# Kernel tuning notes

Measured on AMD Instinct MI355X. Metric: run time of the kernel, lower is better.

The kernel has to match this reference:

```python
import jax, jax.numpy as jnp
import numpy as np
from jax import lax

DIM = 256
NUM_HEADS = 8
HEAD_DIM = DIM // NUM_HEADS
SCALE = HEAD_DIM ** -0.5


def _avg_pool(x, k, p):
    # torch AvgPool2d(kernel=k, stride=1, padding=p) with count_include_pad=True
    s = lax.reduce_window(x, 0.0, lax.add,
                          window_dimensions=(1, 1, k, k),
                          window_strides=(1, 1, 1, 1),
                          padding=((0, 0), (0, 0), (p, p), (p, p)))
    return s / (k * k)


def setup_inputs() -> dict:
    key = jax.random.key(0)
    ks = jax.random.split(key, 7)
    x = jax.random.normal(ks[0], (2, DIM, 48, 48), dtype=jnp.float32)
    q_w = jax.random.normal(ks[1], (DIM, DIM), dtype=jnp.float32) * (DIM ** -0.5)
    q_b = jax.random.normal(ks[2], (DIM,), dtype=jnp.float32) * 0.02
    kv_w = jax.random.normal(ks[3], (2 * DIM, DIM), dtype=jnp.float32) * (DIM ** -0.5)
    kv_b = jax.random.normal(ks[4], (2 * DIM,), dtype=jnp.float32) * 0.02
    proj_w = jax.random.normal(ks[5], (DIM, DIM), dtype=jnp.float32) * (DIM ** -0.5)
    proj_b = jax.random.normal(ks[6], (DIM,), dtype=jnp.float32) * 0.02
    return {"x": x, "q_w": q_w, "q_b": q_b, "kv_w": kv_w, "kv_b": kv_b,
            "proj_w": proj_w, "proj_b": proj_b}


def reference(x, q_w, q_b, kv_w, kv_b, proj_w, proj_b):
    B, C, H, W = x.shape
    h, d, N = NUM_HEADS, HEAD_DIM, H * W

    # q = 1x1 conv -> [B, h, N, d]
    q = jnp.einsum('oc,bchw->bohw', q_w, x) + q_b[None, :, None, None]
    q = q.reshape(B, h, d, N).transpose(0, 1, 3, 2)

    # kv is a linear 1x1 conv, so (kv(x)+kv(p1)+kv(p2)+kv(p3))/4 == kv(mean of inputs)
    x_avg = (x + _avg_pool(x, 3, 1) + _avg_pool(x, 5, 2) + _avg_pool(x, 7, 3)) / 4.0
    kv = jnp.einsum('oc,bchw->bohw', kv_w, x_avg) + kv_b[None, :, None, None]
    kv = kv.reshape(B, 2, h, d, N).transpose(1, 0, 2, 4, 3)  # [2, B, h, N, d]
    k, v = kv[0], kv[1]

    attn = jnp.einsum('bhnd,bhmd->bhnm', q, k) * SCALE  # [B, h, N, N]
    attn = jax.nn.softmax(attn, axis=-1)
    y = jnp.einsum('bhnm,bhmd->bhnd', attn, v)  # [B, h, N, d]
    # faithful to torch: transpose(1,2) then flat reshape to [B, C, H, W]
    y = y.transpose(0, 2, 1, 3).reshape(B, C, H, W)

    out = jnp.einsum('oc,bchw->bohw', proj_w, y) + proj_b[None, :, None, None]
    return out
```

## Files before the change

kernel.cpp:

```cpp
#include <hip/hip_runtime.h>
#include <hip/hip_bf16.h>
#include <cstdint>

#define DIMC  256
#define NH    8
#define HD    32
#define NPIX  2304
#define BATCH 2
#define KT    32
#define NWAVE 4
#define NTW   18
#define KPW   576

typedef short s16x8 __attribute__((ext_vector_type(8)));
typedef short s16x4 __attribute__((ext_vector_type(4)));
typedef float f32x4 __attribute__((ext_vector_type(4)));

#define MFMA32(A,B,C) __builtin_amdgcn_mfma_f32_16x16x32_bf16(A,B,C,0,0,0)

__device__ inline uint32_t rnau(float x) { return __float_as_uint(x) + 0x8000u; }
__device__ inline uint32_t pk2(uint32_t l_, uint32_t h_) {
  return __builtin_amdgcn_perm(h_, l_, 0x07060302u);
}
__device__ inline uint32_t cvtpk(float lo, float hi) {
  uint32_t r;
  asm("v_cvt_pk_bf16_f32 %0, %1, %2" : "=v"(r) : "v"(lo), "v"(hi));
  return r;
}

__global__ __launch_bounds__(256) void pool_kernel(const float* __restrict__ x,
                                                   float* __restrict__ xavg) {
  const int plane = blockIdx.x;
  const float* xp = x + (size_t)plane * NPIX;
  __shared__ float sx[NPIX];
  __shared__ float h3[NPIX], h5[NPIX], h7[NPIX];
  const int t = threadIdx.x;
#pragma unroll
  for (int r = 0; r < 9; ++r) sx[r * 256 + t] = xp[r * 256 + t];
  __syncthreads();
#pragma unroll
  for (int r = 0; r < 9; ++r) {
    int p = r * 256 + t;
    int i = p / 48, j = p - i * 48;
    float a3 = 0.f, a5 = 0.f, a7 = 0.f;
#pragma unroll
    for (int dj = -3; dj <= 3; ++dj) {
      int jj = j + dj;
      if (jj < 0 || jj >= 48) continue;
      float v = sx[i * 48 + jj];
      a7 += v;
      if (dj >= -2 && dj <= 2) a5 += v;
      if (dj >= -1 && dj <= 1) a3 += v;
    }
    h3[p] = a3; h5[p] = a5; h7[p] = a7;
  }
  __syncthreads();
#pragma unroll
  for (int r = 0; r < 9; ++r) {
    int p = r * 256 + t;
    int i = p / 48, j = p - i * 48;
    float b3 = 0.f, b5 = 0.f, b7 = 0.f;
#pragma unroll
    for (int di = -3; di <= 3; ++di) {
      int ii = i + di;
      if (ii < 0 || ii >= 48) continue;
      int q = ii * 48 + j;
      b7 += h7[q];
      if (di >= -2 && di <= 2) b5 += h5[q];
      if (di >= -1 && di <= 1) b3 += h3[q];
    }
    xavg[(size_t)plane * NPIX + p] =
        0.25f * (sx[p] + b3 * (1.f / 9.f) + b5 * (1.f / 25.f) + b7 * (1.f / 49.f));
  }
}

__global__ __launch_bounds__(256) void conv_all(
    const float* __restrict__ x, const float* __restrict__ xavg,
    const float* __restrict__ qw, const float* __restrict__ kvw,
    const float* __restrict__ pw_,
    short* __restrict__ Xh, short* __restrict__ Ah,
    short* __restrict__ Wth) {
  const int bx = blockIdx.x;
  const int t = threadIdx.x;
  if (bx < 576) {
    const float* src = (bx < 288) ? x : xavg;
    short* dhi = (bx < 288) ? Xh : Ah;
    const int bb = (bx < 288) ? bx : bx - 288;
    const int n0 = (bb % 36) * 64, c0 = ((bb / 36) & 3) * 64, b = bb / 144;
    __shared__ __align__(16) float T[64][68];
    {
      const int c = t >> 2, n4 = (t & 3) * 16;
      const float* sp = src + ((size_t)b * DIMC + c0 + c) * NPIX + n0 + n4;
#pragma unroll
      for (int i2 = 0; i2 < 4; ++i2)
        *(f32x4*)&T[c][n4 + i2 * 4] = *(const f32x4*)(sp + i2 * 4);
    }
    __syncthreads();
    {
      const int n = t >> 2, c4 = (t & 3) * 16;
      float v[16];
#pragma unroll
      for (int i = 0; i < 16; ++i) v[i] = T[c4 + i][n];
      uint32_t a[16];
#pragma unroll
      for (int i = 0; i < 16; ++i) a[i] = rnau(v[i]);
      union { s16x8 s; uint32_t u[4]; } H0, H1;
#pragma unroll
      for (int j = 0; j < 4; ++j) {
        H0.u[j] = pk2(a[2 * j], a[2 * j + 1]);
        H1.u[j] = pk2(a[8 + 2 * j], a[8 + 2 * j + 1]);
      }
      const size_t off = ((size_t)b * NPIX + n0 + n) * DIMC + c0 + c4;
      *(s16x8*)(dhi + off) = H0.s; *(s16x8*)(dhi + off + 8) = H1.s;
    }
  } else {
    const int idx = ((bx - 576) * 256 + t) * 8;
    const float* s;
    int off;
    if (idx < 65536)       { s = qw;  off = idx; }
    else if (idx < 196608) { s = kvw; off = idx - 65536; }
    else                   { s = pw_; off = idx - 196608; }
    f32x4 x0 = *(const f32x4*)(s + off);
    f32x4 x1 = *(const f32x4*)(s + off + 4);
    float v[8] = {x0[0], x0[1], x0[2], x0[3], x1[0], x1[1], x1[2], x1[3]};
    uint32_t a[8];
#pragma unroll
    for (int i = 0; i < 8; ++i) a[i] = rnau(v[i]);
    union { s16x8 s; uint32_t u[4]; } H;
#pragma unroll
    for (int j = 0; j < 4; ++j) H.u[j] = pk2(a[2 * j], a[2 * j + 1]);
    *(s16x8*)(Wth + idx) = H.s;
  }
}

__global__ __launch_bounds__(128) void gemm_qkv_hi(
    const short* __restrict__ Wth,
    const float* __restrict__ q_b, const float* __restrict__ kv_b,
    const short* __restrict__ Xh, const short* __restrict__ Ah,
    short* __restrict__ Qhi, short* __restrict__ Khi, short* __restrict__ Vhi,
    float qscale) {
  __shared__ __align__(16) float Cl[64][68];
  const int by = blockIdx.y;
  const bool isQ = (by < 4);
  const int o0 = isQ ? by * 64 : (by - 4) * 64;
  const short* Wh = isQ ? Wth : Wth + 65536;
  const float* bias = isQ ? q_b : kv_b;
  const short* Inh = isQ ? Xh : Ah;
  const float scale = isQ ? qscale : 1.0f;
  short* d1 = isQ ? Qhi : Khi;
  const int n0 = blockIdx.x * 64;
  const int b  = blockIdx.z;

  const int tid = threadIdx.x;
  const int wave = tid >> 6, lane = tid & 63;
  const int g = lane >> 4, q = lane & 15;

  const short* wph = Wh + ((o0 + wave * 32 + q) * DIMC + g * 8);
  const short* iph = Inh + ((size_t)(b * NPIX + n0 + q) * DIMC + g * 8);

  f32x4 acc[2][4] = {{{0,0,0,0},{0,0,0,0},{0,0,0,0},{0,0,0,0}},
                     {{0,0,0,0},{0,0,0,0},{0,0,0,0},{0,0,0,0}}};
#pragma unroll
  for (int c0 = 0; c0 < DIMC; c0 += 32) {
    s16x8 a0 = *(const s16x8*)(wph + c0);
    s16x8 a1 = *(const s16x8*)(wph + 16 * DIMC + c0);
#pragma unroll
    for (int st = 0; st < 4; ++st) {
      s16x8 bh_ = *(const s16x8*)(iph + (size_t)st * 16 * DIMC + c0);
      acc[0][st] = MFMA32(a0, bh_, acc[0][st]);
      acc[1][st] = MFMA32(a1, bh_, acc[1][st]);
    }
  }
#pragma unroll
  for (int a16 = 0; a16 < 2; ++a16)
#pragma unroll
    for (int st = 0; st < 4; ++st)
#pragma unroll
      for (int r = 0; r < 4; ++r)
        Cl[wave * 32 + a16 * 16 + g * 4 + r][st * 16 + q] = acc[a16][st][r];
  __syncthreads();

  if (by < 8) {
    const int n = tid >> 1, oq = tid & 1;
#pragma unroll
    for (int h2 = 0; h2 < 2; ++h2) {
      const int h = (o0 >> 5) + h2;
      const float* bp = bias + o0 + h2 * 32 + oq * 16;
      float v[16];
#pragma unroll
      for (int i = 0; i < 16; ++i)
        v[i] = (Cl[h2 * 32 + oq * 16 + i][n] + bp[i]) * scale;
      uint32_t a[16];
#pragma unroll
      for (int i = 0; i < 16; ++i) a[i] = rnau(v[i]);
      union { s16x8 s; uint32_t u[4]; } H0, H1;
#pragma unroll
      for (int j = 0; j < 4; ++j) {
        H0.u[j] = pk2(a[2 * j], a[2 * j + 1]);
        H1.u[j] = pk2(a[8 + 2 * j], a[8 + 2 * j + 1]);
      }
      const size_t off = ((size_t)((b * 8 + h) * NPIX + n0 + n)) * HD + oq * 16;
      *(s16x8*)(d1 + off) = H0.s; *(s16x8*)(d1 + off + 8) = H1.s;
    }
  } else {
    const int o = tid >> 2, nc = (tid & 3) * 16;
#pragma unroll
    for (int h2 = 0; h2 < 2; ++h2) {
      const int ch = o0 + h2 * 32 + o;
      const int h = (ch - 256) >> 5;
      const float bv = bias[ch];
      float v[16];
#pragma unroll
      for (int i2 = 0; i2 < 4; ++i2) {
        f32x4 t4 = *(const f32x4*)&Cl[h2 * 32 + o][nc + i2 * 4];
        v[i2 * 4 + 0] = t4[0] + bv; v[i2 * 4 + 1] = t4[1] + bv;
        v[i2 * 4 + 2] = t4[2] + bv; v[i2 * 4 + 3] = t4[3] + bv;
      }
      uint32_t a[16];
#pragma unroll
      for (int i = 0; i < 16; ++i) a[i] = rnau(v[i]);
      short* po = Vhi + ((size_t)((b * 8 + h) * HD + o)) * NPIX + n0 + (nc & 32);
      const int phase = (nc & 16) ? 4 : 0;
#pragma unroll
      for (int j = 0; j < 4; ++j) {
        uint2 wv;
        wv.x = pk2(a[4 * j], a[4 * j + 1]);
        wv.y = pk2(a[4 * j + 2], a[4 * j + 3]);
        *(uint2*)(po + phase + 8 * j) = wv;
      }
    }
  }
}

__global__ __launch_bounds__(256) void attn_fused(
    const short* __restrict__ Qhi,
    const short* __restrict__ Khi,
    const short* __restrict__ Vhi,
    short* __restrict__ zh) {
  const int li = blockIdx.x;
  const int r144 = li >> 3;
  const int bh = 2 * (li & 7) + (r144 >= 72 ? 1 : 0);
  const int qb = (r144 >= 72) ? r144 - 72 : r144;
  const int tid = threadIdx.x;
  const int wave = tid >> 6, lane = tid & 63;
  const int g = lane >> 4, q = lane & 15;
  const int base = qb * 32;

  __shared__ __align__(16) float R[4][64][20];

  const size_t qoff = ((size_t)bh * NPIX + base + q) * HD + g * 8;
  const s16x8 qhA = *(const s16x8*)(Qhi + qoff);
  const s16x8 qhB = *(const s16x8*)(Qhi + qoff + 16 * HD);

  const short* kp = Khi + ((size_t)bh * NPIX + wave * KPW + q) * HD + g * 8;
  const short* vp = Vhi + ((size_t)bh * HD + q) * NPIX + wave * KPW + g * 8;

  const f32x4 Z4 = {0.f, 0.f, 0.f, 0.f};
  f32x4 OA0 = Z4, OA1 = Z4, OB0 = Z4, OB1 = Z4;
  f32x4 LA = Z4, LB = Z4;
  s16x8 kb[3][2], vb[3][2], pfA, pfB, vp0, vp1;

  union { s16x8 s; uint32_t u[4]; } ONE, ZZ;
  ONE.u[0] = 0x3F803F80u; ONE.u[1] = 0x3F803F80u;
  ONE.u[2] = 0x3F803F80u; ONE.u[3] = 0x3F803F80u;
  ZZ.u[0] = 0; ZZ.u[1] = 0; ZZ.u[2] = 0; ZZ.u[3] = 0;
  const s16x8 ones = ONE.s;
  pfA = ZZ.s; pfB = ZZ.s;
  vp0 = ones; vp1 = ones;

  kb[0][0] = *(const s16x8*)(kp);
  kb[0][1] = *(const s16x8*)(kp + 16 * HD);
  vb[0][0] = *(const s16x8*)(vp);
  vb[0][1] = *(const s16x8*)(vp + 16 * NPIX);
  kb[1][0] = *(const s16x8*)(kp + KT * HD);
  kb[1][1] = *(const s16x8*)(kp + KT * HD + 16 * HD);
  vb[1][0] = *(const s16x8*)(vp + KT);
  vb[1][1] = *(const s16x8*)(vp + KT + 16 * NPIX);

#define ATTN_STEP(CUR, NX2, T)                                                \
  {                                                                           \
    if ((T) + 2 < NTW) {                                                      \
      const short* kpn = kp + ((T) + 2) * (KT * HD);                          \
      const short* vpn = vp + ((T) + 2) * KT;                                 \
      kb[NX2][0] = *(const s16x8*)(kpn);                                      \
      kb[NX2][1] = *(const s16x8*)(kpn + 16 * HD);                            \
      vb[NX2][0] = *(const s16x8*)(vpn);                                      \
      vb[NX2][1] = *(const s16x8*)(vpn + 16 * NPIX);                          \
    }                                                                         \
    f32x4 SA0 = MFMA32(kb[CUR][0], qhA, Z4);                                  \
    f32x4 SA1 = MFMA32(kb[CUR][1], qhA, Z4);                                  \
    f32x4 SB0 = MFMA32(kb[CUR][0], qhB, Z4);                                  \
    f32x4 SB1 = MFMA32(kb[CUR][1], qhB, Z4);                                  \
    OA0 = MFMA32(vp0, pfA, OA0);                                              \
    OA1 = MFMA32(vp1, pfA, OA1);                                              \
    OB0 = MFMA32(vp0, pfB, OB0);                                              \
    OB1 = MFMA32(vp1, pfB, OB1);                                              \
    LA  = MFMA32(ones, pfA, LA);                                              \
    LB  = MFMA32(ones, pfB, LB);                                              \
    {                                                                         \
      union { s16x8 s; uint32_t u[4]; } PA;                                   \
      PA.u[0] = cvtpk(exp2f(SA0[0]), exp2f(SA0[1]));                          \
      PA.u[1] = cvtpk(exp2f(SA0[2]), exp2f(SA0[3]));                          \
      PA.u[2] = cvtpk(exp2f(SA1[0]), exp2f(SA1[1]));                          \
      PA.u[3] = cvtpk(exp2f(SA1[2]), exp2f(SA1[3]));                          \
      pfA = PA.s;                                                             \
    }                                                                         \
    {                                                                         \
      union { s16x8 s; uint32_t u[4]; } PB;                                   \
      PB.u[0] = cvtpk(exp2f(SB0[0]), exp2f(SB0[1]));                          \
      PB.u[1] = cvtpk(exp2f(SB0[2]), exp2f(SB0[3]));                          \
      PB.u[2] = cvtpk(exp2f(SB1[0]), exp2f(SB1[1]));                          \
      PB.u[3] = cvtpk(exp2f(SB1[2]), exp2f(SB1[3]));                          \
      pfB = PB.s;                                                             \
    }                                                                         \
    vp0 = vb[CUR][0]; vp1 = vb[CUR][1];                                       \
  }

#pragma unroll 1
  for (int tt = 0; tt < NTW; tt += 3) {
    ATTN_STEP(0, 2, tt);
    ATTN_STEP(1, 0, tt + 1);
    ATTN_STEP(2, 1, tt + 2);
  }
#undef ATTN_STEP

  OA0 = MFMA32(vp0, pfA, OA0);
  OA1 = MFMA32(vp1, pfA, OA1);
  OB0 = MFMA32(vp0, pfB, OB0);
  OB1 = MFMA32(vp1, pfB, OB1);
  LA  = MFMA32(ones, pfA, LA);
  LB  = MFMA32(ones, pfB, LB);

  {
    float* rw = &R[wave][lane][0];
    *(f32x4*)&rw[0]  = OA0;
    *(f32x4*)&rw[4]  = OA1;
    *(f32x4*)&rw[8]  = OB0;
    *(f32x4*)&rw[12] = OB1;
    rw[16] = LA[0];
    rw[17] = LB[0];
  }
  __syncthreads();
  {
    const int l2 = tid & 63, eg = tid >> 6;
    const int g2 = l2 >> 4, q2 = l2 & 15;
    f32x4 s = {0.f, 0.f, 0.f, 0.f};
    float Lt = 0.f;
#pragma unroll
    for (int w = 0; w < NWAVE; ++w) {
      const f32x4 pv = *(const f32x4*)&R[w][l2][eg * 4];
      s[0] += pv[0]; s[1] += pv[1]; s[2] += pv[2]; s[3] += pv[3];
      Lt += R[w][l2][16 + (eg >> 1)];
    }
    const float inv = 1.f / Lt;
    const int h = bh & 7, b = bh >> 3;
    const int n = base + ((eg & 2) ? 16 : 0) + q2;
    const int d0 = ((eg & 1) ? 16 : 0) + g2 * 4;
    const int c = n / 9, r = n - c * 9;
    short* zp = zh + ((size_t)(b * NPIX + r * 256 + h * HD + d0)) * DIMC + c;
#pragma unroll
    for (int j = 0; j < 4; ++j)
      zp[(size_t)j * DIMC] = (short)(rnau(s[j] * inv) >> 16);
  }
}

__global__ __launch_bounds__(128) void gemm_proj_hi(
    const short* __restrict__ Wh,
    const float* __restrict__ bias,
    const short* __restrict__ Zh,
    float* __restrict__ out) {
  __shared__ __align__(16) float Cl[64][68];
  const int n0 = blockIdx.x * 64;
  const int o0 = blockIdx.y * 64;
  const int b  = blockIdx.z;
  const int tid = threadIdx.x;
  const int wave = tid >> 6, lane = tid & 63;
  const int g = lane >> 4, q = lane & 15;

  const short* wph = Wh + ((o0 + wave * 32 + q) * DIMC + g * 8);
  const short* iph = Zh + ((size_t)(b * NPIX + n0 + q) * DIMC + g * 8);

  f32x4 acc[2][4] = {{{0,0,0,0},{0,0,0,0},{0,0,0,0},{0,0,0,0}},
                     {{0,0,0,0},{0,0,0,0},{0,0,0,0},{0,0,0,0}}};
#pragma unroll
  for (int c0 = 0; c0 < DIMC; c0 += 32) {
    s16x8 a0 = *(const s16x8*)(wph + c0);
    s16x8 a1 = *(const s16x8*)(wph + 16 * DIMC + c0);
#pragma unroll
    for (int st = 0; st < 4; ++st) {
      s16x8 bh_ = *(const s16x8*)(iph + (size_t)st * 16 * DIMC + c0);
      acc[0][st] = MFMA32(a0, bh_, acc[0][st]);
      acc[1][st] = MFMA32(a1, bh_, acc[1][st]);
    }
  }
#pragma unroll
  for (int a16 = 0; a16 < 2; ++a16)
#pragma unroll
    for (int st = 0; st < 4; ++st)
#pragma unroll
      for (int r = 0; r < 4; ++r)
        Cl[wave * 32 + a16 * 16 + g * 4 + r][st * 16 + q] = acc[a16][st][r];
  __syncthreads();

  const int o = tid >> 2, nc = (tid & 3) * 16;
#pragma unroll
  for (int h2 = 0; h2 < 2; ++h2) {
    const int row = h2 * 32 + o;
    const float bv = bias[o0 + row];
    float* op = out + ((size_t)b * DIMC + o0 + row) * NPIX + n0 + nc;
#pragma unroll
    for (int i2 = 0; i2 < 4; ++i2) {
      f32x4 v = *(const f32x4*)&Cl[row][nc + i2 * 4];
      v[0] += bv; v[1] += bv; v[2] += bv; v[3] += bv;
      *(f32x4*)(op + i2 * 4) = v;
    }
  }
}

extern "C" void kernel_launch(void* const* d_in, const int* in_sizes, int n_in,
                              void* d_out, int out_size, void* d_ws, size_t ws_size,
                              hipStream_t stream) {
  const float* x      = (const float*)d_in[0];
  const float* q_w    = (const float*)d_in[1];
  const float* q_b    = (const float*)d_in[2];
  const float* kv_w   = (const float*)d_in[3];
  const float* kv_b   = (const float*)d_in[4];
  const float* proj_w = (const float*)d_in[5];
  const float* proj_b = (const float*)d_in[6];
  float* out = (float*)d_out;

  char* w = (char*)d_ws;
  float* xavg = (float*)w;
  short* Xh   = (short*)(w + 4718592);
  short* Ah   = (short*)(w + 9437184);
  short* Wth  = (short*)(w + 28311552);
  short* Qhi  = (short*)(w + 29360128);
  short* Khi  = (short*)(w + 31719424);
  short* Vhi  = (short*)(w + 34078720);
  short* Zh   = (short*)(w + 37322752);

  const float qscale = 0.17677669529663689f * 1.4426950408889634f;

  pool_kernel<<<BATCH * DIMC, 256, 0, stream>>>(x, xavg);
  conv_all<<<704, 256, 0, stream>>>(x, xavg, q_w, kv_w, proj_w, Xh, Ah, Wth);
  gemm_qkv_hi<<<dim3(36, 12, 2), 128, 0, stream>>>(Wth, q_b, kv_b,
                                                   Xh, Ah, Qhi, Khi, Vhi, qscale);
  attn_fused<<<1152, 256, 0, stream>>>(Qhi, Khi, Vhi, Zh);
  gemm_proj_hi<<<dim3(36, 4, 2), 128, 0, stream>>>(Wth + 196608, proj_b, Zh, out);
}
```

Baseline: 141.8 us.

## Process 64 queries per attention block to double K/V reuse

The attention kernel now gives each block 64 query rows instead of 32, with four query fragments per wave. Each loaded K/V tile therefore feeds twice as many MFMAs, halving K/V global traffic, and the grid shrinks from 1152 to 576 blocks. The P packing changes from inline-asm v_cvt_pk_bf16_f32 to a manual round-and-permute sequence. The cost is higher register pressure, more LDS for the cross-wave reduction, and fewer blocks to spread across the CUs.

```diff
diff --git a/kernel.cpp b/kernel.cpp
--- a/kernel.cpp
+++ b/kernel.cpp
@@ -21,11 +21,6 @@
 __device__ inline uint32_t rnau(float x) { return __float_as_uint(x) + 0x8000u; }
 __device__ inline uint32_t pk2(uint32_t l_, uint32_t h_) {
   return __builtin_amdgcn_perm(h_, l_, 0x07060302u);
-}
-__device__ inline uint32_t cvtpk(float lo, float hi) {
-  uint32_t r;
-  asm("v_cvt_pk_bf16_f32 %0, %1, %2" : "=v"(r) : "v"(lo), "v"(hi));
-  return r;
 }
 
 __global__ __launch_bounds__(256) void pool_kernel(const float* __restrict__ x,
@@ -238,34 +233,37 @@
     const short* __restrict__ Vhi,
     short* __restrict__ zh) {
   const int li = blockIdx.x;
-  const int r144 = li >> 3;
-  const int bh = 2 * (li & 7) + (r144 >= 72 ? 1 : 0);
-  const int qb = (r144 >= 72) ? r144 - 72 : r144;
+  const int r72 = li >> 3;
+  const int bh = 2 * (li & 7) + (r72 >= 36 ? 1 : 0);
+  const int qb = (r72 >= 36) ? r72 - 36 : r72;
   const int tid = threadIdx.x;
   const int wave = tid >> 6, lane = tid & 63;
   const int g = lane >> 4, q = lane & 15;
-  const int base = qb * 32;
-
-  __shared__ __align__(16) float R[4][64][20];
+  const int base = qb * 64;
+
+  __shared__ __align__(16) float R[4][64][36];
 
   const size_t qoff = ((size_t)bh * NPIX + base + q) * HD + g * 8;
   const s16x8 qhA = *(const s16x8*)(Qhi + qoff);
   const s16x8 qhB = *(const s16x8*)(Qhi + qoff + 16 * HD);
+  const s16x8 qhC = *(const s16x8*)(Qhi + qoff + 32 * HD);
+  const s16x8 qhD = *(const s16x8*)(Qhi + qoff + 48 * HD);
 
   const short* kp = Khi + ((size_t)bh * NPIX + wave * KPW + q) * HD + g * 8;
   const short* vp = Vhi + ((size_t)bh * HD + q) * NPIX + wave * KPW + g * 8;
 
   const f32x4 Z4 = {0.f, 0.f, 0.f, 0.f};
   f32x4 OA0 = Z4, OA1 = Z4, OB0 = Z4, OB1 = Z4;
-  f32x4 LA = Z4, LB = Z4;
-  s16x8 kb[3][2], vb[3][2], pfA, pfB, vp0, vp1;
+  f32x4 OC0 = Z4, OC1 = Z4, OD0 = Z4, OD1 = Z4;
+  f32x4 LA = Z4, LB = Z4, LC = Z4, LD = Z4;
+  s16x8 kb[3][2], vb[3][2], pfA, pfB, pfC, pfD, vp0, vp1;
 
   union { s16x8 s; uint32_t u[4]; } ONE, ZZ;
   ONE.u[0] = 0x3F803F80u; ONE.u[1] = 0x3F803F80u;
   ONE.u[2] = 0x3F803F80u; ONE.u[3] = 0x3F803F80u;
   ZZ.u[0] = 0; ZZ.u[1] = 0; ZZ.u[2] = 0; ZZ.u[3] = 0;
   const s16x8 ones = ONE.s;
-  pfA = ZZ.s; pfB = ZZ.s;
+  pfA = ZZ.s; pfB = ZZ.s; pfC = ZZ.s; pfD = ZZ.s;
   vp0 = ones; vp1 = ones;
 
   kb[0][0] = *(const s16x8*)(kp);
@@ -276,6 +274,21 @@
   kb[1][1] = *(const s16x8*)(kp + KT * HD + 16 * HD);
   vb[1][0] = *(const s16x8*)(vp + KT);
   vb[1][1] = *(const s16x8*)(vp + KT + 16 * NPIX);
+
+#define PACK_P(PF, S0, S1)                                                    \
+    {                                                                         \
+      f32x4 p0, p1;                                                           \
+      p0[0] = exp2f(S0[0]); p0[1] = exp2f(S0[1]);                             \
+      p0[2] = exp2f(S0[2]); p0[3] = exp2f(S0[3]);                             \
+      p1[0] = exp2f(S1[0]); p1[1] = exp2f(S1[1]);                             \
+      p1[2] = exp2f(S1[2]); p1[3] = exp2f(S1[3]);                             \
+      union { s16x8 s; uint32_t u[4]; } PP;                                   \
+      PP.u[0] = pk2(rnau(p0[0]), rnau(p0[1]));                                \
+      PP.u[1] = pk2(rnau(p0[2]), rnau(p0[3]));                                \
+      PP.u[2] = pk2(rnau(p1[0]), rnau(p1[1]));                                \
+      PP.u[3] = pk2(rnau(p1[2]), rnau(p1[3]));                                \
+      PF = PP.s;                                                              \
+    }
 
 #define ATTN_STEP(CUR, NX2, T)                                                \
   {                                                                           \
@@ -291,28 +304,26 @@
     f32x4 SA1 = MFMA32(kb[CUR][1], qhA, Z4);                                  \
     f32x4 SB0 = MFMA32(kb[CUR][0], qhB, Z4);                                  \
     f32x4 SB1 = MFMA32(kb[CUR][1], qhB, Z4);                                  \
+    f32x4 SC0 = MFMA32(kb[CUR][0], qhC, Z4);                                  \
+    f32x4 SC1 = MFMA32(kb[CUR][1], qhC, Z4);                                  \
+    f32x4 SD0 = MFMA32(kb[CUR][0], qhD, Z4);                                  \
+    f32x4 SD1 = MFMA32(kb[CUR][1], qhD, Z4);                                  \
     OA0 = MFMA32(vp0, pfA, OA0);                                              \
     OA1 = MFMA32(vp1, pfA, OA1);                                              \
     OB0 = MFMA32(vp0, pfB, OB0);                                              \
     OB1 = MFMA32(vp1, pfB, OB1);                                              \
+    OC0 = MFMA32(vp0, pfC, OC0);                                              \
+    OC1 = MFMA32(vp1, pfC, OC1);                                              \
+    OD0 = MFMA32(vp0, pfD, OD0);                                              \
+    OD1 = MFMA32(vp1, pfD, OD1);                                              \
     LA  = MFMA32(ones, pfA, LA);                                              \
     LB  = MFMA32(ones, pfB, LB);                                              \
-    {                                                                         \
-      union { s16x8 s; uint32_t u[4]; } PA;                                   \
-      PA.u[0] = cvtpk(exp2f(SA0[0]), exp2f(SA0[1]));                          \
-      PA.u[1] = cvtpk(exp2f(SA0[2]), exp2f(SA0[3]));                          \
-      PA.u[2] = cvtpk(exp2f(SA1[0]), exp2f(SA1[1]));                          \
-      PA.u[3] = cvtpk(exp2f(SA1[2]), exp2f(SA1[3]));                          \
-      pfA = PA.s;                                                             \
-    }                                                                         \
-    {                                                                         \
-      union { s16x8 s; uint32_t u[4]; } PB;                                   \
-      PB.u[0] = cvtpk(exp2f(SB0[0]), exp2f(SB0[1]));                          \
-      PB.u[1] = cvtpk(exp2f(SB0[2]), exp2f(SB0[3]));                          \
-      PB.u[2] = cvtpk(exp2f(SB1[0]), exp2f(SB1[1]));                          \
-      PB.u[3] = cvtpk(exp2f(SB1[2]), exp2f(SB1[3]));                          \
-      pfB = PB.s;                                                             \
-    }                                                                         \
+    LC  = MFMA32(ones, pfC, LC);                                              \
+    LD  = MFMA32(ones, pfD, LD);                                              \
+    PACK_P(pfA, SA0, SA1)                                                     \
+    PACK_P(pfB, SB0, SB1)                                                     \
+    PACK_P(pfC, SC0, SC1)                                                     \
+    PACK_P(pfD, SD0, SD1)                                                     \
     vp0 = vb[CUR][0]; vp1 = vb[CUR][1];                                       \
   }
 
@@ -323,13 +334,20 @@
     ATTN_STEP(2, 1, tt + 2);
   }
 #undef ATTN_STEP
+#undef PACK_P
 
   OA0 = MFMA32(vp0, pfA, OA0);
   OA1 = MFMA32(vp1, pfA, OA1);
   OB0 = MFMA32(vp0, pfB, OB0);
   OB1 = MFMA32(vp1, pfB, OB1);
+  OC0 = MFMA32(vp0, pfC, OC0);
+  OC1 = MFMA32(vp1, pfC, OC1);
+  OD0 = MFMA32(vp0, pfD, OD0);
+  OD1 = MFMA32(vp1, pfD, OD1);
   LA  = MFMA32(ones, pfA, LA);
   LB  = MFMA32(ones, pfB, LB);
+  LC  = MFMA32(ones, pfC, LC);
+  LD  = MFMA32(ones, pfD, LD);
 
   {
     float* rw = &R[wave][lane][0];
@@ -337,30 +355,42 @@
     *(f32x4*)&rw[4]  = OA1;
     *(f32x4*)&rw[8]  = OB0;
     *(f32x4*)&rw[12] = OB1;
-    rw[16] = LA[0];
-    rw[17] = LB[0];
+    *(f32x4*)&rw[16] = OC0;
+    *(f32x4*)&rw[20] = OC1;
+    *(f32x4*)&rw[24] = OD0;
+    *(f32x4*)&rw[28] = OD1;
+    rw[32] = LA[0];
+    rw[33] = LB[0];
+    rw[34] = LC[0];
+    rw[35] = LD[0];
   }
   __syncthreads();
   {
     const int l2 = tid & 63, eg = tid >> 6;
     const int g2 = l2 >> 4, q2 = l2 & 15;
-    f32x4 s = {0.f, 0.f, 0.f, 0.f};
+    f32x4 s0 = {0.f, 0.f, 0.f, 0.f};
+    f32x4 s1 = {0.f, 0.f, 0.f, 0.f};
     float Lt = 0.f;
 #pragma unroll
     for (int w = 0; w < NWAVE; ++w) {
-      const f32x4 pv = *(const f32x4*)&R[w][l2][eg * 4];
-      s[0] += pv[0]; s[1] += pv[1]; s[2] += pv[2]; s[3] += pv[3];
-      Lt += R[w][l2][16 + (eg >> 1)];
+      const float* rw = &R[w][l2][0];
+      const f32x4 a0 = *(const f32x4*)&rw[eg * 8];
+      const f32x4 a1 = *(const f32x4*)&rw[eg * 8 + 4];
+      s0[0] += a0[0]; s0[1] += a0[1]; s0[2] += a0[2]; s0[3] += a0[3];
+      s1[0] += a1[0]; s1[1] += a1[1]; s1[2] += a1[2]; s1[3] += a1[3];
+      Lt += rw[32 + eg];
     }
     const float inv = 1.f / Lt;
     const int h = bh & 7, b = bh >> 3;
-    const int n = base + ((eg & 2) ? 16 : 0) + q2;
-    const int d0 = ((eg & 1) ? 16 : 0) + g2 * 4;
+    const int n = base + eg * 16 + q2;
     const int c = n / 9, r = n - c * 9;
-    short* zp = zh + ((size_t)(b * NPIX + r * 256 + h * HD + d0)) * DIMC + c;
-#pragma unroll
-    for (int j = 0; j < 4; ++j)
-      zp[(size_t)j * DIMC] = (short)(rnau(s[j] * inv) >> 16);
+    short* zp0 = zh + ((size_t)(b * NPIX + r * 256 + h * HD + g2 * 4)) * DIMC + c;
+    short* zp1 = zp0 + (size_t)16 * DIMC;
+#pragma unroll
+    for (int j = 0; j < 4; ++j) {
+      zp0[(size_t)j * DIMC] = (short)(rnau(s0[j] * inv) >> 16);
+      zp1[(size_t)j * DIMC] = (short)(rnau(s1[j] * inv) >> 16);
+    }
   }
 }
 
@@ -445,6 +475,6 @@
   conv_all<<<704, 256, 0, stream>>>(x, xavg, q_w, kv_w, proj_w, Xh, Ah, Wth);
   gemm_qkv_hi<<<dim3(36, 12, 2), 128, 0, stream>>>(Wth, q_b, kv_b,
                                                    Xh, Ah, Qhi, Khi, Vhi, qscale);
-  attn_fused<<<1152, 256, 0, stream>>>(Qhi, Khi, Vhi, Zh);
+  attn_fused<<<576, 256, 0, stream>>>(Qhi, Khi, Vhi, Zh);
   gemm_proj_hi<<<dim3(36, 4, 2), 128, 0, stream>>>(Wth + 196608, proj_b, Zh, out);
 }
```

Measured after the change: 145.6 us. 2.7% more time.
